# Optimization experiments

Hardware: AMD Instinct MI355X
Metric: run time of the kernel (lower is better)

The kernel has to match this reference:

```python
import jax, jax.numpy as jnp
import numpy as np

N_SEG, N_REG, N_EDGE, HID, CHEB_K = 40000, 1000, 640000, 256, 5


def setup_inputs() -> dict:
    key = jax.random.key(0)
    ks = jax.random.split(key, 6)
    return {
        "projected_region_features": jax.random.normal(ks[0], (N_REG, HID), jnp.float32),
        "segment2region_assignment": jax.random.uniform(ks[1], (N_SEG, N_REG), jnp.float32),
        "edge_index": jax.random.randint(ks[2], (2, N_EDGE), 0, N_SEG, dtype=jnp.int64),
        # ChebConv params: one [HID,HID] weight per Chebyshev order + shared bias
        "cheb_W": jax.random.normal(ks[3], (CHEB_K, HID, HID), jnp.float32) / np.sqrt(HID).astype(np.float32),
        "cheb_b": jnp.zeros((HID,), jnp.float32),
        "ln_gamma": jnp.ones((HID,), jnp.float32),
        "ln_beta": jnp.zeros((HID,), jnp.float32),
    }


def _cheb_conv(x, edge_index, W, b):
    """PyG ChebConv with normalization='sym', lambda_max=2.0.
    Scaled Laplacian L_hat = 2L/lam - I = -D^{-1/2} A D^{-1/2} (diag = 0)."""
    N = x.shape[0]
    src, dst = edge_index[0], edge_index[1]
    w = (src != dst).astype(x.dtype)  # remove_self_loops
    deg = jax.ops.segment_sum(w, src, num_segments=N)
    dinv = jnp.where(deg > 0, jax.lax.rsqrt(jnp.where(deg > 0, deg, 1.0)), 0.0)
    norm = -w * dinv[src] * dinv[dst]  # per-edge weight of L_hat

    def prop(t):  # y_i = sum_{(j->i)} norm_e * t_j
        return jax.ops.segment_sum(norm[:, None] * t[src], dst, num_segments=N)

    Tx0 = x
    out = Tx0 @ W[0]
    Tx1 = prop(Tx0)
    out = out + Tx1 @ W[1]
    for k in range(2, W.shape[0]):
        Tx2 = 2.0 * prop(Tx1) - Tx0
        out = out + Tx2 @ W[k]
        Tx0, Tx1 = Tx1, Tx2
    return out + b


def _layer_norm(x, g, b, eps=1e-5):
    mu = jnp.mean(x, axis=-1, keepdims=True)
    var = jnp.mean(jnp.square(x - mu), axis=-1, keepdims=True)
    return (x - mu) * jax.lax.rsqrt(var + eps) * g + b


def reference(projected_region_features, segment2region_assignment, edge_index,
              cheb_W, cheb_b, ln_gamma, ln_beta):
    # [n_seg, n_reg] @ [n_reg, hid] -> [n_seg, hid]
    seg_low_raw = segment2region_assignment @ projected_region_features
    seg_low = _cheb_conv(seg_low_raw, edge_index, cheb_W, cheb_b)
    seg_low = _layer_norm(jax.nn.gelu(seg_low, approximate=False), ln_gamma, ln_beta)
    return (seg_low, seg_low_raw)
```

## Files before the change

kernel.cpp:

```cpp
#include <hip/hip_runtime.h>

#define NSEG 40000
#define NREG 1000
#define NEDGE 640000
#define HID 256
#define KCAT 1280
#define KP1 1024
#define LPAD 40
#define NBLK 157

typedef float f32x4 __attribute__((ext_vector_type(4)));
typedef float f32x2 __attribute__((ext_vector_type(2)));
typedef short s16x8 __attribute__((ext_vector_type(8)));
typedef unsigned short u16x4 __attribute__((ext_vector_type(4)));
typedef unsigned short u16x8 __attribute__((ext_vector_type(8)));
typedef unsigned int u32x2 __attribute__((ext_vector_type(2)));

typedef __attribute__((address_space(3))) unsigned int lds_u32;
typedef __attribute__((address_space(1))) const unsigned int glb_u32;

__device__ __forceinline__ void dma16(const void* g, void* l) {
    __builtin_amdgcn_global_load_lds((glb_u32*)g, (lds_u32*)l, 16, 0, 0);
}

__device__ __forceinline__ unsigned short f2bf(float f) {
    unsigned u = __builtin_bit_cast(unsigned, f);
    u += 0x7FFFu + ((u >> 16) & 1u);
    return (unsigned short)(u >> 16);
}
__device__ __forceinline__ float bf2f(unsigned short h) {
    unsigned u = ((unsigned)h) << 16;
    return __builtin_bit_cast(float, u);
}
__device__ __forceinline__ unsigned char f2fp8(float v) {
    return (unsigned char)__builtin_amdgcn_cvt_pk_fp8_f32(v, v, 0, false);
}

__device__ __forceinline__ f32x4 mfma16(s16x8 a, s16x8 b, f32x4 c) {
    return __builtin_amdgcn_mfma_f32_16x16x32_bf16(a, b, c, 0, 0, 0);
}

__global__ void detect_kernel(const unsigned int* __restrict__ E, int* flag) {
    int lane = threadIdx.x;
    unsigned v = E[2 * lane + 1];
    unsigned long long m = __ballot(v == 0u);
    if (lane == 0) *flag = (__popcll(m) >= 48) ? 1 : 0;
}

__device__ __forceinline__ int edge_at(const void* E, int idx, int is64) {
    return is64 ? (int)((const long long*)E)[idx] : ((const int*)E)[idx];
}

__global__ __launch_bounds__(256) void deg_cnt_kernel(const void* __restrict__ E,
                                                      const int* __restrict__ flag,
                                                      int* deg, int* cnt) {
    int e = blockIdx.x * 256 + threadIdx.x;
    if (e >= NEDGE) return;
    int is64 = *flag;
    int s = edge_at(E, e, is64);
    int d = edge_at(E, e + NEDGE, is64);
    if (s != d) {
        atomicAdd(&deg[s], 1);
        atomicAdd(&cnt[d], 1);
    }
}

__global__ __launch_bounds__(256) void scan1_kernel(const int* __restrict__ cnt,
                                                    const int* __restrict__ deg,
                                                    float* __restrict__ dinv,
                                                    int* __restrict__ bsum) {
    __shared__ int sh[256];
    int t = threadIdx.x;
    int i = blockIdx.x * 256 + t;
    int c = (i < NSEG) ? cnt[i] : 0;
    sh[t] = c;
    if (i < NSEG) {
        int d = deg[i];
        dinv[i] = d > 0 ? rsqrtf((float)d) : 0.f;
    }
    __syncthreads();
    for (int o = 128; o > 0; o >>= 1) {
        if (t < o) sh[t] += sh[t + o];
        __syncthreads();
    }
    if (t == 0) bsum[blockIdx.x] = sh[0];
}

__global__ __launch_bounds__(256) void scan2_kernel(const int* __restrict__ bsum,
                                                    int* __restrict__ boff,
                                                    int* __restrict__ rowptr) {
    __shared__ int sh[256];
    int t = threadIdx.x;
    int v = (t < NBLK) ? bsum[t] : 0;
    sh[t] = v;
    __syncthreads();
    for (int o = 1; o < 256; o <<= 1) {
        int x = 0;
        if (t >= o) x = sh[t - o];
        __syncthreads();
        if (t >= o) sh[t] += x;
        __syncthreads();
    }
    if (t < NBLK) boff[t] = sh[t] - v;
    if (t == 255) rowptr[NSEG] = sh[255];
}

__global__ __launch_bounds__(256) void scan3_kernel(const int* __restrict__ cnt,
                                                    const int* __restrict__ boff,
                                                    int* __restrict__ rowptr,
                                                    int* __restrict__ cursor) {
    __shared__ int sh[256];
    int t = threadIdx.x;
    int i = blockIdx.x * 256 + t;
    int v = (i < NSEG) ? cnt[i] : 0;
    sh[t] = v;
    __syncthreads();
    for (int o = 1; o < 256; o <<= 1) {
        int x = 0;
        if (t >= o) x = sh[t - o];
        __syncthreads();
        if (t >= o) sh[t] += x;
        __syncthreads();
    }
    if (i < NSEG) {
        int p = boff[blockIdx.x] + sh[t] - v;
        rowptr[i] = p;
        cursor[i] = p;
    }
}

__global__ __launch_bounds__(256) void scatter_kernel(const void* __restrict__ E,
                                                      const int* __restrict__ flag,
                                                      const float* __restrict__ dinv,
                                                      int* cursor,
                                                      long long* __restrict__ colval) {
    int e = blockIdx.x * 256 + threadIdx.x;
    if (e >= NEDGE) return;
    int is64 = *flag;
    int s = edge_at(E, e, is64);
    int d = edge_at(E, e + NEDGE, is64);
    if (s != d) {
        int pos = atomicAdd(&cursor[d], 1);
        float v = -dinv[s] * dinv[d];
        colval[pos] = ((long long)(unsigned)__builtin_bit_cast(unsigned, v) << 32)
                    | (unsigned)s;
    }
}

__global__ void prep_w_kernel(const float* __restrict__ P, const float* __restrict__ W,
                              unsigned short* __restrict__ Pt, unsigned short* __restrict__ Wt) {
    int n = blockIdx.x;
    for (int k = threadIdx.x; k < KP1; k += blockDim.x)
        Pt[(size_t)n * KP1 + k] = (k < NREG) ? f2bf(P[(size_t)k * HID + n]) : (unsigned short)0;
    for (int k = threadIdx.x; k < KCAT; k += blockDim.x)
        Wt[(size_t)n * KCAT + k] = f2bf(W[(size_t)k * HID + n]);
}

__global__ __launch_bounds__(256) void gemm1_kernel(const float* __restrict__ S,
                                                    const unsigned short* __restrict__ Pt,
                                                    float* __restrict__ raw,
                                                    unsigned short* __restrict__ xcat,
                                                    unsigned char* __restrict__ x8) {
    __shared__ unsigned short As[64][LPAD];
    __shared__ unsigned short Bs[256][LPAD];
    const int m0 = blockIdx.x * 64;
    const int tid = threadIdx.x;
    const int lane = tid & 63, wn = tid >> 6;
    const int r = lane & 15, q = lane >> 4;
    const int srow = tid >> 2, scol = (tid & 3) * 8;

    f32x4 acc[4][4] = {};

    for (int kb = 0; kb < NREG; kb += 32) {
        const bool kvalid = (kb + scol + 8 <= NREG);
        u16x8 av = {0, 0, 0, 0, 0, 0, 0, 0};
        u16x8 bv0 = av, bv1 = av, bv2 = av, bv3 = av;
        if (kvalid) {
            const float* sp = S + (size_t)(m0 + srow) * NREG + kb + scol;
            f32x4 f0 = *(const f32x4*)sp;
            f32x4 f1 = *(const f32x4*)(sp + 4);
            av[0] = f2bf(f0[0]); av[1] = f2bf(f0[1]); av[2] = f2bf(f0[2]); av[3] = f2bf(f0[3]);
            av[4] = f2bf(f1[0]); av[5] = f2bf(f1[1]); av[6] = f2bf(f1[2]); av[7] = f2bf(f1[3]);
            bv0 = *(const u16x8*)(Pt + (size_t)(srow)       * KP1 + kb + scol);
            bv1 = *(const u16x8*)(Pt + (size_t)(srow +  64) * KP1 + kb + scol);
            bv2 = *(const u16x8*)(Pt + (size_t)(srow + 128) * KP1 + kb + scol);
            bv3 = *(const u16x8*)(Pt + (size_t)(srow + 192) * KP1 + kb + scol);
        }
        __syncthreads();
        *(u16x8*)&As[srow][scol] = av;
        *(u16x8*)&Bs[srow][scol] = bv0;
        *(u16x8*)&Bs[srow + 64][scol] = bv1;
        *(u16x8*)&Bs[srow + 128][scol] = bv2;
        *(u16x8*)&Bs[srow + 192][scol] = bv3;
        __syncthreads();
        s16x8 af[4], bfv[4];
#pragma unroll
        for (int am = 0; am < 4; ++am) af[am] = *(const s16x8*)&As[am * 16 + r][q * 8];
#pragma unroll
        for (int bn = 0; bn < 4; ++bn) bfv[bn] = *(const s16x8*)&Bs[wn * 64 + bn * 16 + r][q * 8];
#pragma unroll
        for (int am = 0; am < 4; ++am) {
#pragma unroll
            for (int bn = 0; bn < 4; ++bn)
                acc[am][bn] = mfma16(af[am], bfv[bn], acc[am][bn]);
        }
    }
#pragma unroll
    for (int am = 0; am < 4; ++am) {
        int rowb = m0 + am * 16 + q * 4;
#pragma unroll
        for (int bn = 0; bn < 4; ++bn) {
            int col = wn * 64 + bn * 16 + r;
#pragma unroll
            for (int i = 0; i < 4; ++i) {
                float v = acc[am][bn][i];
                raw[(size_t)(rowb + i) * HID + col] = v;
                xcat[(size_t)(rowb + i) * KCAT + col] = f2bf(v);
                x8[(size_t)(rowb + i) * KCAT + col] = f2fp8(v);
            }
        }
    }
}

__global__ __launch_bounds__(256) void prop_kernel(unsigned short* xcat,
                                                   unsigned char* x8,
                                                   const int* __restrict__ rowptr,
                                                   const long long* __restrict__ colval,
                                                   int inOff, int outOff, int subOff,
                                                   float scale, int writeFp8) {
    const int g = blockIdx.x * 4 + (threadIdx.x >> 6);
    const int lane = threadIdx.x & 63;
    const int half = lane >> 5;
    const int l5 = lane & 31;
    const int e0 = rowptr[g], e1 = rowptr[g + 1];
    float a0 = 0.f, a1 = 0.f, a2 = 0.f, a3 = 0.f;
    float a4 = 0.f, a5 = 0.f, a6 = 0.f, a7 = 0.f;
    const unsigned char* xin = x8 + inOff + l5 * 8;

    for (int base = e0; base < e1; base += 64) {
        int m = e1 - base;
        if (m > 64) m = 64;
        int cc = 0;
        float vv = 0.f;
        if (lane < m) {
            long long cv = colval[base + lane];
            cc = (int)(unsigned)cv;
            vv = __builtin_bit_cast(float, (unsigned)(cv >> 32));
        }
        int i = 0;
#pragma unroll 4
        for (; i + 2 <= m; i += 2) {
            int c = __shfl(cc, i + half);
            float v = __shfl(vv, i + half);
            u32x2 t = *(const u32x2*)(xin + (size_t)c * KCAT);
            f32x2 d0 = __builtin_amdgcn_cvt_pk_f32_fp8(t[0], false);
            f32x2 d1 = __builtin_amdgcn_cvt_pk_f32_fp8(t[0], true);
            f32x2 d2 = __builtin_amdgcn_cvt_pk_f32_fp8(t[1], false);
            f32x2 d3 = __builtin_amdgcn_cvt_pk_f32_fp8(t[1], true);
            a0 += v * d0[0]; a1 += v * d0[1];
            a2 += v * d1[0]; a3 += v * d1[1];
            a4 += v * d2[0]; a5 += v * d2[1];
            a6 += v * d3[0]; a7 += v * d3[1];
        }
        if (i < m) {
            int c = __shfl(cc, i);
            float v = __shfl(vv, i);
            if (half == 0) {
                u32x2 t = *(const u32x2*)(xin + (size_t)c * KCAT);
                f32x2 d0 = __builtin_amdgcn_cvt_pk_f32_fp8(t[0], false);
                f32x2 d1 = __builtin_amdgcn_cvt_pk_f32_fp8(t[0], true);
                f32x2 d2 = __builtin_amdgcn_cvt_pk_f32_fp8(t[1], false);
                f32x2 d3 = __builtin_amdgcn_cvt_pk_f32_fp8(t[1], true);
                a0 += v * d0[0]; a1 += v * d0[1];
                a2 += v * d1[0]; a3 += v * d1[1];
                a4 += v * d2[0]; a5 += v * d2[1];
                a6 += v * d3[0]; a7 += v * d3[1];
            }
        }
    }
    a0 += __shfl_xor(a0, 32); a1 += __shfl_xor(a1, 32);
    a2 += __shfl_xor(a2, 32); a3 += __shfl_xor(a3, 32);
    a4 += __shfl_xor(a4, 32); a5 += __shfl_xor(a5, 32);
    a6 += __shfl_xor(a6, 32); a7 += __shfl_xor(a7, 32);

    if (half == 0) {
        a0 *= scale; a1 *= scale; a2 *= scale; a3 *= scale;
        a4 *= scale; a5 *= scale; a6 *= scale; a7 *= scale;
        if (subOff >= 0) {
            u16x8 p = *(const u16x8*)(xcat + (size_t)g * KCAT + subOff + l5 * 8);
            a0 -= bf2f(p[0]); a1 -= bf2f(p[1]); a2 -= bf2f(p[2]); a3 -= bf2f(p[3]);
            a4 -= bf2f(p[4]); a5 -= bf2f(p[5]); a6 -= bf2f(p[6]); a7 -= bf2f(p[7]);
        }
        u16x8 o = {f2bf(a0), f2bf(a1), f2bf(a2), f2bf(a3),
                   f2bf(a4), f2bf(a5), f2bf(a6), f2bf(a7)};
        *(u16x8*)(xcat + (size_t)g * KCAT + outOff + l5 * 8) = o;
        if (writeFp8) {
            unsigned p0 = 0, p1 = 0;
            p0 = __builtin_amdgcn_cvt_pk_fp8_f32(a0, a1, (int)p0, false);
            p0 = __builtin_amdgcn_cvt_pk_fp8_f32(a2, a3, (int)p0, true);
            p1 = __builtin_amdgcn_cvt_pk_fp8_f32(a4, a5, (int)p1, false);
            p1 = __builtin_amdgcn_cvt_pk_fp8_f32(a6, a7, (int)p1, true);
            u32x2 o8 = {p0, p1};
            *(u32x2*)(x8 + (size_t)g * KCAT + outOff + l5 * 8) = o8;
        }
    }
}

__global__ __launch_bounds__(512) void gemm2_kernel(const unsigned short* __restrict__ xcat,
                                                    const unsigned short* __restrict__ Wt,
                                                    const float* __restrict__ bias,
                                                    const float* __restrict__ gamma,
                                                    const float* __restrict__ beta,
                                                    float* __restrict__ outp) {
    __shared__ unsigned short As[2][128 * 32];
    __shared__ unsigned short Bs[2][256 * 32];
    __shared__ float rs[128][4];
    __shared__ float rss[128][4];
    const int tid = threadIdx.x;
    const int lane = tid & 63, wid = tid >> 6;
    const int wm = wid >> 2, wn = wid & 3;
    const int r = lane & 15, q = lane >> 4;
    const int qx8 = (q ^ (r & 3)) << 3;
    const int m0 = blockIdx.x * 128;
    const int crow = lane >> 2;
    const int bcol = (((lane & 3) ^ ((lane >> 2) & 3)) << 3);

    f32x4 acc[4][4] = {};

    auto stage = [&](int c, int kb) {
#pragma unroll
        for (int k = 0; k < 3; ++k) {
            int idx = 3 * wid + k;
            if (idx < 16) {
                int n = idx * 16 + crow;
                dma16(Wt + (size_t)n * KCAT + kb + bcol, &Bs[c][idx * 512]);
            } else {
                int a = idx - 16;
                int row = m0 + a * 16 + crow;
                dma16(xcat + (size_t)row * KCAT + kb + bcol, &As[c][a * 512]);
            }
        }
    };

    stage(0, 0);
    __syncthreads();

    for (int t = 0; t < 40; ++t) {
        const int c = t & 1;
        if (t < 39) stage(c ^ 1, (t + 1) * 32);
        s16x8 af[4], bfv[4];
#pragma unroll
        for (int am = 0; am < 4; ++am)
            af[am] = *(const s16x8*)&As[c][(wm * 64 + am * 16 + r) * 32 + qx8];
#pragma unroll
        for (int bn = 0; bn < 4; ++bn)
            bfv[bn] = *(const s16x8*)&Bs[c][(wn * 64 + bn * 16 + r) * 32 + qx8];
#pragma unroll
        for (int am = 0; am < 4; ++am)
#pragma unroll
            for (int bn = 0; bn < 4; ++bn)
                acc[am][bn] = mfma16(af[am], bfv[bn], acc[am][bn]);
        __syncthreads();
    }

    float bc[4], gm[4], bt[4];
#pragma unroll
    for (int bn = 0; bn < 4; ++bn) {
        int col = wn * 64 + bn * 16 + r;
        bc[bn] = bias[col];
        gm[bn] = gamma[col];
        bt[bn] = beta[col];
    }
#pragma unroll
    for (int am = 0; am < 4; ++am) {
#pragma unroll
        for (int i = 0; i < 4; ++i) {
            float s = 0.f, ss = 0.f;
#pragma unroll
            for (int bn = 0; bn < 4; ++bn) {
                float v = acc[am][bn][i] + bc[bn];
                v = 0.5f * v * (1.f + erff(v * 0.70710678118654752f));
                acc[am][bn][i] = v;
                s += v;
                ss += v * v;
            }
#pragma unroll
            for (int msk = 1; msk < 16; msk <<= 1) {
                s += __shfl_xor(s, msk);
                ss += __shfl_xor(ss, msk);
            }
            if (r == 0) {
                int row = wm * 64 + am * 16 + q * 4 + i;
                rs[row][wn] = s;
                rss[row][wn] = ss;
            }
        }
    }
    __syncthreads();
#pragma unroll
    for (int am = 0; am < 4; ++am) {
#pragma unroll
        for (int i = 0; i < 4; ++i) {
            int row = wm * 64 + am * 16 + q * 4 + i;
            float s = rs[row][0] + rs[row][1] + rs[row][2] + rs[row][3];
            float ss = rss[row][0] + rss[row][1] + rss[row][2] + rss[row][3];
            float mu = s * (1.f / HID);
            float var = ss * (1.f / HID) - mu * mu;
            float inv = rsqrtf(var + 1e-5f);
            if (m0 + row < NSEG) {
#pragma unroll
                for (int bn = 0; bn < 4; ++bn) {
                    int col = wn * 64 + bn * 16 + r;
                    outp[(size_t)(m0 + row) * HID + col] = (acc[am][bn][i] - mu) * inv * gm[bn] + bt[bn];
                }
            }
        }
    }
}

extern "C" void kernel_launch(void* const* d_in, const int* in_sizes, int n_in,
                              void* d_out, int out_size, void* d_ws, size_t ws_size,
                              hipStream_t stream) {
    const float* P     = (const float*)d_in[0];
    const float* S     = (const float*)d_in[1];
    const void*  E     = d_in[2];
    const float* W     = (const float*)d_in[3];
    const float* bias  = (const float*)d_in[4];
    const float* gamma = (const float*)d_in[5];
    const float* beta  = (const float*)d_in[6];

    float* out = (float*)d_out;
    float* raw = out + (size_t)NSEG * HID;

    char* ws = (char*)d_ws;
    size_t off = 0;
    auto alloc = [&](size_t bytes) -> void* {
        void* p = ws + off;
        off += (bytes + 255) & ~(size_t)255;
        return p;
    };
    unsigned short* xcat   = (unsigned short*)alloc((size_t)NSEG * KCAT * 2);
    unsigned char*  x8     = (unsigned char*)alloc((size_t)NSEG * KCAT);
    unsigned short* Pt     = (unsigned short*)alloc((size_t)HID * KP1 * 2);
    unsigned short* Wt     = (unsigned short*)alloc((size_t)HID * KCAT * 2);
    int*            deg    = (int*)alloc((size_t)NSEG * 4);
    float*          dinv   = (float*)alloc((size_t)NSEG * 4);
    int*            cnt    = (int*)alloc((size_t)NSEG * 4);
    int*            rowptr = (int*)alloc((size_t)(NSEG + 1) * 4);
    int*            cursor = (int*)alloc((size_t)NSEG * 4);
    long long*      colval = (long long*)alloc((size_t)NEDGE * 8);
    int*            bsum   = (int*)alloc((size_t)NBLK * 4);
    int*            boff   = (int*)alloc((size_t)NBLK * 4);
    int*            flag   = (int*)alloc(256);
    if (off > ws_size) return;

    hipMemsetAsync(deg, 0, (size_t)NSEG * 4, stream);
    hipMemsetAsync(cnt, 0, (size_t)NSEG * 4, stream);

    detect_kernel<<<1, 64, 0, stream>>>((const unsigned int*)E, flag);
    prep_w_kernel<<<HID, 256, 0, stream>>>(P, W, Pt, Wt);

    deg_cnt_kernel<<<NEDGE / 256, 256, 0, stream>>>(E, flag, deg, cnt);
    scan1_kernel<<<NBLK, 256, 0, stream>>>(cnt, deg, dinv, bsum);
    scan2_kernel<<<1, 256, 0, stream>>>(bsum, boff, rowptr);
    scan3_kernel<<<NBLK, 256, 0, stream>>>(cnt, boff, rowptr, cursor);
    scatter_kernel<<<NEDGE / 256, 256, 0, stream>>>(E, flag, dinv, cursor, colval);

    gemm1_kernel<<<NSEG / 64, 256, 0, stream>>>(S, Pt, raw, xcat, x8);

    prop_kernel<<<NSEG / 4, 256, 0, stream>>>(xcat, x8, rowptr, colval, 0 * HID, 1 * HID, -1, 1.f, 1);
    prop_kernel<<<NSEG / 4, 256, 0, stream>>>(xcat, x8, rowptr, colval, 1 * HID, 2 * HID, 0 * HID, 2.f, 1);
    prop_kernel<<<NSEG / 4, 256, 0, stream>>>(xcat, x8, rowptr, colval, 2 * HID, 3 * HID, 1 * HID, 2.f, 1);
    prop_kernel<<<NSEG / 4, 256, 0, stream>>>(xcat, x8, rowptr, colval, 3 * HID, 4 * HID, 2 * HID, 2.f, 0);

    gemm2_kernel<<<(NSEG + 127) / 128, 512, 0, stream>>>(xcat, Wt, bias, gamma, beta, out);
}
```

Before: 385.5 us.

## Run final Chebyshev GEMM in FP8 using fp8 activations and weights

The output GEMM over the concatenated Chebyshev features now reads FP8 copies of the activations and weights and uses the fp8 16x16x32 MFMA instead of bf16. The last propagation step now also writes an FP8 copy, and prep_w builds an FP8 transposed weight matrix. The LDS staging layout changes to 32-byte rows without the XOR swizzle. This halves the GEMM's global and LDS traffic and uses the faster FP8 matrix path. In exchange, accuracy drops because activations and weights are quantized to FP8, which risks tolerance failures, and the unswizzled LDS reads may hit bank conflicts.

```diff
diff --git a/kernel.cpp b/kernel.cpp
--- a/kernel.cpp
+++ b/kernel.cpp
@@ -38,6 +38,9 @@
 
 __device__ __forceinline__ f32x4 mfma16(s16x8 a, s16x8 b, f32x4 c) {
     return __builtin_amdgcn_mfma_f32_16x16x32_bf16(a, b, c, 0, 0, 0);
+}
+__device__ __forceinline__ f32x4 mfma8(long a, long b, f32x4 c) {
+    return __builtin_amdgcn_mfma_f32_16x16x32_fp8_fp8(a, b, c, 0, 0, 0);
 }
 
 __global__ void detect_kernel(const unsigned int* __restrict__ E, int* flag) {
@@ -148,12 +151,16 @@
 }
 
 __global__ void prep_w_kernel(const float* __restrict__ P, const float* __restrict__ W,
-                              unsigned short* __restrict__ Pt, unsigned short* __restrict__ Wt) {
+                              unsigned short* __restrict__ Pt, unsigned short* __restrict__ Wt,
+                              unsigned char* __restrict__ Wt8) {
     int n = blockIdx.x;
     for (int k = threadIdx.x; k < KP1; k += blockDim.x)
         Pt[(size_t)n * KP1 + k] = (k < NREG) ? f2bf(P[(size_t)k * HID + n]) : (unsigned short)0;
-    for (int k = threadIdx.x; k < KCAT; k += blockDim.x)
-        Wt[(size_t)n * KCAT + k] = f2bf(W[(size_t)k * HID + n]);
+    for (int k = threadIdx.x; k < KCAT; k += blockDim.x) {
+        float w = W[(size_t)k * HID + n];
+        Wt[(size_t)n * KCAT + k] = f2bf(w);
+        Wt8[(size_t)n * KCAT + k] = f2fp8(w);
+    }
 }
 
 __global__ __launch_bounds__(256) void gemm1_kernel(const float* __restrict__ S,
@@ -227,7 +234,7 @@
                                                    const int* __restrict__ rowptr,
                                                    const long long* __restrict__ colval,
                                                    int inOff, int outOff, int subOff,
-                                                   float scale, int writeFp8) {
+                                                   float scale) {
     const int g = blockIdx.x * 4 + (threadIdx.x >> 6);
     const int lane = threadIdx.x & 63;
     const int half = lane >> 5;
@@ -294,51 +301,44 @@
         u16x8 o = {f2bf(a0), f2bf(a1), f2bf(a2), f2bf(a3),
                    f2bf(a4), f2bf(a5), f2bf(a6), f2bf(a7)};
         *(u16x8*)(xcat + (size_t)g * KCAT + outOff + l5 * 8) = o;
-        if (writeFp8) {
-            unsigned p0 = 0, p1 = 0;
-            p0 = __builtin_amdgcn_cvt_pk_fp8_f32(a0, a1, (int)p0, false);
-            p0 = __builtin_amdgcn_cvt_pk_fp8_f32(a2, a3, (int)p0, true);
-            p1 = __builtin_amdgcn_cvt_pk_fp8_f32(a4, a5, (int)p1, false);
-            p1 = __builtin_amdgcn_cvt_pk_fp8_f32(a6, a7, (int)p1, true);
-            u32x2 o8 = {p0, p1};
-            *(u32x2*)(x8 + (size_t)g * KCAT + outOff + l5 * 8) = o8;
-        }
-    }
-}
-
-__global__ __launch_bounds__(512) void gemm2_kernel(const unsigned short* __restrict__ xcat,
-                                                    const unsigned short* __restrict__ Wt,
+        unsigned p0 = 0, p1 = 0;
+        p0 = __builtin_amdgcn_cvt_pk_fp8_f32(a0, a1, (int)p0, false);
+        p0 = __builtin_amdgcn_cvt_pk_fp8_f32(a2, a3, (int)p0, true);
+        p1 = __builtin_amdgcn_cvt_pk_fp8_f32(a4, a5, (int)p1, false);
+        p1 = __builtin_amdgcn_cvt_pk_fp8_f32(a6, a7, (int)p1, true);
+        u32x2 o8 = {p0, p1};
+        *(u32x2*)(x8 + (size_t)g * KCAT + outOff + l5 * 8) = o8;
+    }
+}
+
+__global__ __launch_bounds__(512) void gemm2_kernel(const unsigned char* __restrict__ x8,
+                                                    const unsigned char* __restrict__ Wt8,
                                                     const float* __restrict__ bias,
                                                     const float* __restrict__ gamma,
                                                     const float* __restrict__ beta,
                                                     float* __restrict__ outp) {
-    __shared__ unsigned short As[2][128 * 32];
-    __shared__ unsigned short Bs[2][256 * 32];
+    __shared__ unsigned char As8[2][128 * 32];
+    __shared__ unsigned char Bs8[2][256 * 32];
     __shared__ float rs[128][4];
     __shared__ float rss[128][4];
     const int tid = threadIdx.x;
     const int lane = tid & 63, wid = tid >> 6;
     const int wm = wid >> 2, wn = wid & 3;
     const int r = lane & 15, q = lane >> 4;
-    const int qx8 = (q ^ (r & 3)) << 3;
     const int m0 = blockIdx.x * 128;
-    const int crow = lane >> 2;
-    const int bcol = (((lane & 3) ^ ((lane >> 2) & 3)) << 3);
+    const int drow = lane >> 1;
+    const int dhalf = (lane & 1) * 16;
 
     f32x4 acc[4][4] = {};
 
     auto stage = [&](int c, int kb) {
-#pragma unroll
-        for (int k = 0; k < 3; ++k) {
-            int idx = 3 * wid + k;
-            if (idx < 16) {
-                int n = idx * 16 + crow;
-                dma16(Wt + (size_t)n * KCAT + kb + bcol, &Bs[c][idx * 512]);
-            } else {
-                int a = idx - 16;
-                int row = m0 + a * 16 + crow;
-                dma16(xcat + (size_t)row * KCAT + kb + bcol, &As[c][a * 512]);
-            }
+        {
+            int n = wid * 32 + drow;
+            dma16(Wt8 + (size_t)n * KCAT + kb + dhalf, &Bs8[c][wid * 1024]);
+        }
+        if (wid < 4) {
+            int row = m0 + wid * 32 + drow;
+            dma16(x8 + (size_t)row * KCAT + kb + dhalf, &As8[c][wid * 1024]);
         }
     };
 
@@ -348,18 +348,18 @@
     for (int t = 0; t < 40; ++t) {
         const int c = t & 1;
         if (t < 39) stage(c ^ 1, (t + 1) * 32);
-        s16x8 af[4], bfv[4];
+        long af[4], bfv[4];
 #pragma unroll
         for (int am = 0; am < 4; ++am)
-            af[am] = *(const s16x8*)&As[c][(wm * 64 + am * 16 + r) * 32 + qx8];
+            af[am] = *(const long*)&As8[c][(wm * 64 + am * 16 + r) * 32 + q * 8];
 #pragma unroll
         for (int bn = 0; bn < 4; ++bn)
-            bfv[bn] = *(const s16x8*)&Bs[c][(wn * 64 + bn * 16 + r) * 32 + qx8];
+            bfv[bn] = *(const long*)&Bs8[c][(wn * 64 + bn * 16 + r) * 32 + q * 8];
 #pragma unroll
         for (int am = 0; am < 4; ++am)
 #pragma unroll
             for (int bn = 0; bn < 4; ++bn)
-                acc[am][bn] = mfma16(af[am], bfv[bn], acc[am][bn]);
+                acc[am][bn] = mfma8(af[am], bfv[bn], acc[am][bn]);
         __syncthreads();
     }
 
@@ -443,6 +443,7 @@
     unsigned char*  x8     = (unsigned char*)alloc((size_t)NSEG * KCAT);
     unsigned short* Pt     = (unsigned short*)alloc((size_t)HID * KP1 * 2);
     unsigned short* Wt     = (unsigned short*)alloc((size_t)HID * KCAT * 2);
+    unsigned char*  Wt8    = (unsigned char*)alloc((size_t)HID * KCAT);
     int*            deg    = (int*)alloc((size_t)NSEG * 4);
     float*          dinv   = (float*)alloc((size_t)NSEG * 4);
     int*            cnt    = (int*)alloc((size_t)NSEG * 4);
@@ -458,7 +459,7 @@
     hipMemsetAsync(cnt, 0, (size_t)NSEG * 4, stream);
 
     detect_kernel<<<1, 64, 0, stream>>>((const unsigned int*)E, flag);
-    prep_w_kernel<<<HID, 256, 0, stream>>>(P, W, Pt, Wt);
+    prep_w_kernel<<<HID, 256, 0, stream>>>(P, W, Pt, Wt, Wt8);
 
     deg_cnt_kernel<<<NEDGE / 256, 256, 0, stream>>>(E, flag, deg, cnt);
     scan1_kernel<<<NBLK, 256, 0, stream>>>(cnt, deg, dinv, bsum);
@@ -468,10 +469,10 @@
 
     gemm1_kernel<<<NSEG / 64, 256, 0, stream>>>(S, Pt, raw, xcat, x8);
 
-    prop_kernel<<<NSEG / 4, 256, 0, stream>>>(xcat, x8, rowptr, colval, 0 * HID, 1 * HID, -1, 1.f, 1);
-    prop_kernel<<<NSEG / 4, 256, 0, stream>>>(xcat, x8, rowptr, colval, 1 * HID, 2 * HID, 0 * HID, 2.f, 1);
-    prop_kernel<<<NSEG / 4, 256, 0, stream>>>(xcat, x8, rowptr, colval, 2 * HID, 3 * HID, 1 * HID, 2.f, 1);
-    prop_kernel<<<NSEG / 4, 256, 0, stream>>>(xcat, x8, rowptr, colval, 3 * HID, 4 * HID, 2 * HID, 2.f, 0);
-
-    gemm2_kernel<<<(NSEG + 127) / 128, 512, 0, stream>>>(xcat, Wt, bias, gamma, beta, out);
-}
+    prop_kernel<<<NSEG / 4, 256, 0, stream>>>(xcat, x8, rowptr, colval, 0 * HID, 1 * HID, -1, 1.f);
+    prop_kernel<<<NSEG / 4, 256, 0, stream>>>(xcat, x8, rowptr, colval, 1 * HID, 2 * HID, 0 * HID, 2.f);
+    prop_kernel<<<NSEG / 4, 256, 0, stream>>>(xcat, x8, rowptr, colval, 2 * HID, 3 * HID, 1 * HID, 2.f);
+    prop_kernel<<<NSEG / 4, 256, 0, stream>>>(xcat, x8, rowptr, colval, 3 * HID, 4 * HID, 2 * HID, 2.f);
+
+    gemm2_kernel<<<(NSEG + 127) / 128, 512, 0, stream>>>(x8, Wt8, bias, gamma, beta, out);
+}
```

After: 390.4 us. Within noise of the previous version (+1.3%).

## Switch Chebyshev combine GEMM to FP8 MFMA and widen GEMM1 K-step

Applied to the files above, without the earlier changes.

The final concatenated GEMM now reads FP8 activations and FP8 weights, using the 16x16x32 fp8 MFMA with 64-wide K tiles and a swizzled LDS layout. This halves the operand bytes loaded per output tile and the number of K iterations. The prop kernels now always write FP8 and only write bf16 where a later subtraction needs it, which cuts store traffic. GEMM1 processes 64 K-columns per barrier pair instead of 32. The cost is lower accuracy, since FP8 weights and activations feed a LayerNorm output, and a tail-clamping trick that reads index 0 for out-of-range K, relying on the zero padding in Pt to cancel those terms.

```diff
diff --git a/kernel.cpp b/kernel.cpp
--- a/kernel.cpp
+++ b/kernel.cpp
@@ -6,7 +6,7 @@
 #define HID 256
 #define KCAT 1280
 #define KP1 1024
-#define LPAD 40
+#define LP2 72
 #define NBLK 157
 
 typedef float f32x4 __attribute__((ext_vector_type(4)));
@@ -38,6 +38,9 @@
 
 __device__ __forceinline__ f32x4 mfma16(s16x8 a, s16x8 b, f32x4 c) {
     return __builtin_amdgcn_mfma_f32_16x16x32_bf16(a, b, c, 0, 0, 0);
+}
+__device__ __forceinline__ f32x4 mfma8(long a, long b, f32x4 c) {
+    return __builtin_amdgcn_mfma_f32_16x16x32_fp8_fp8(a, b, c, 0, 0, 0);
 }
 
 __global__ void detect_kernel(const unsigned int* __restrict__ E, int* flag) {
@@ -148,12 +151,12 @@
 }
 
 __global__ void prep_w_kernel(const float* __restrict__ P, const float* __restrict__ W,
-                              unsigned short* __restrict__ Pt, unsigned short* __restrict__ Wt) {
+                              unsigned short* __restrict__ Pt, unsigned char* __restrict__ Wt8) {
     int n = blockIdx.x;
     for (int k = threadIdx.x; k < KP1; k += blockDim.x)
         Pt[(size_t)n * KP1 + k] = (k < NREG) ? f2bf(P[(size_t)k * HID + n]) : (unsigned short)0;
     for (int k = threadIdx.x; k < KCAT; k += blockDim.x)
-        Wt[(size_t)n * KCAT + k] = f2bf(W[(size_t)k * HID + n]);
+        Wt8[(size_t)n * KCAT + k] = f2fp8(W[(size_t)k * HID + n]);
 }
 
 __global__ __launch_bounds__(256) void gemm1_kernel(const float* __restrict__ S,
@@ -161,49 +164,64 @@
                                                     float* __restrict__ raw,
                                                     unsigned short* __restrict__ xcat,
                                                     unsigned char* __restrict__ x8) {
-    __shared__ unsigned short As[64][LPAD];
-    __shared__ unsigned short Bs[256][LPAD];
+    __shared__ unsigned short As[64][LP2];
+    __shared__ unsigned short Bs[256][LP2];
     const int m0 = blockIdx.x * 64;
     const int tid = threadIdx.x;
     const int lane = tid & 63, wn = tid >> 6;
     const int r = lane & 15, q = lane >> 4;
-    const int srow = tid >> 2, scol = (tid & 3) * 8;
+    const int srow = tid >> 2, scol = (tid & 3) * 16;
+    const float* aptr = S + (size_t)(m0 + srow) * NREG;
 
     f32x4 acc[4][4] = {};
 
-    for (int kb = 0; kb < NREG; kb += 32) {
-        const bool kvalid = (kb + scol + 8 <= NREG);
-        u16x8 av = {0, 0, 0, 0, 0, 0, 0, 0};
-        u16x8 bv0 = av, bv1 = av, bv2 = av, bv3 = av;
-        if (kvalid) {
-            const float* sp = S + (size_t)(m0 + srow) * NREG + kb + scol;
-            f32x4 f0 = *(const f32x4*)sp;
-            f32x4 f1 = *(const f32x4*)(sp + 4);
-            av[0] = f2bf(f0[0]); av[1] = f2bf(f0[1]); av[2] = f2bf(f0[2]); av[3] = f2bf(f0[3]);
-            av[4] = f2bf(f1[0]); av[5] = f2bf(f1[1]); av[6] = f2bf(f1[2]); av[7] = f2bf(f1[3]);
-            bv0 = *(const u16x8*)(Pt + (size_t)(srow)       * KP1 + kb + scol);
-            bv1 = *(const u16x8*)(Pt + (size_t)(srow +  64) * KP1 + kb + scol);
-            bv2 = *(const u16x8*)(Pt + (size_t)(srow + 128) * KP1 + kb + scol);
-            bv3 = *(const u16x8*)(Pt + (size_t)(srow + 192) * KP1 + kb + scol);
-        }
-        __syncthreads();
-        *(u16x8*)&As[srow][scol] = av;
-        *(u16x8*)&Bs[srow][scol] = bv0;
-        *(u16x8*)&Bs[srow + 64][scol] = bv1;
-        *(u16x8*)&Bs[srow + 128][scol] = bv2;
-        *(u16x8*)&Bs[srow + 192][scol] = bv3;
-        __syncthreads();
-        s16x8 af[4], bfv[4];
-#pragma unroll
-        for (int am = 0; am < 4; ++am) af[am] = *(const s16x8*)&As[am * 16 + r][q * 8];
-#pragma unroll
-        for (int bn = 0; bn < 4; ++bn) bfv[bn] = *(const s16x8*)&Bs[wn * 64 + bn * 16 + r][q * 8];
+    for (int kb = 0; kb < KP1; kb += 64) {
+        int ka0 = kb + scol;     if (ka0 + 8 > NREG) ka0 = 0;
+        int ka1 = kb + scol + 8; if (ka1 + 8 > NREG) ka1 = 0;
+        f32x4 f0 = *(const f32x4*)(aptr + ka0);
+        f32x4 f1 = *(const f32x4*)(aptr + ka0 + 4);
+        f32x4 f2 = *(const f32x4*)(aptr + ka1);
+        f32x4 f3 = *(const f32x4*)(aptr + ka1 + 4);
+        u16x8 bv[4][2];
+#pragma unroll
+        for (int j = 0; j < 4; ++j) {
+            const unsigned short* bp = Pt + (size_t)(j * 64 + srow) * KP1 + kb + scol;
+            bv[j][0] = *(const u16x8*)(bp);
+            bv[j][1] = *(const u16x8*)(bp + 8);
+        }
+        __syncthreads();
+        {
+            u16x8 a0 = {f2bf(f0[0]), f2bf(f0[1]), f2bf(f0[2]), f2bf(f0[3]),
+                        f2bf(f1[0]), f2bf(f1[1]), f2bf(f1[2]), f2bf(f1[3])};
+            u16x8 a1 = {f2bf(f2[0]), f2bf(f2[1]), f2bf(f2[2]), f2bf(f2[3]),
+                        f2bf(f3[0]), f2bf(f3[1]), f2bf(f3[2]), f2bf(f3[3])};
+            *(u16x8*)&As[srow][scol] = a0;
+            *(u16x8*)&As[srow][scol + 8] = a1;
+        }
+#pragma unroll
+        for (int j = 0; j < 4; ++j) {
+            *(u16x8*)&Bs[j * 64 + srow][scol] = bv[j][0];
+            *(u16x8*)&Bs[j * 64 + srow][scol + 8] = bv[j][1];
+        }
+        __syncthreads();
+        s16x8 af[4][2], bfv[4][2];
 #pragma unroll
         for (int am = 0; am < 4; ++am) {
-#pragma unroll
-            for (int bn = 0; bn < 4; ++bn)
-                acc[am][bn] = mfma16(af[am], bfv[bn], acc[am][bn]);
-        }
+            af[am][0] = *(const s16x8*)&As[am * 16 + r][q * 8];
+            af[am][1] = *(const s16x8*)&As[am * 16 + r][32 + q * 8];
+        }
+#pragma unroll
+        for (int bn = 0; bn < 4; ++bn) {
+            bfv[bn][0] = *(const s16x8*)&Bs[wn * 64 + bn * 16 + r][q * 8];
+            bfv[bn][1] = *(const s16x8*)&Bs[wn * 64 + bn * 16 + r][32 + q * 8];
+        }
+#pragma unroll
+        for (int kk = 0; kk < 2; ++kk)
+#pragma unroll
+            for (int am = 0; am < 4; ++am)
+#pragma unroll
+                for (int bn = 0; bn < 4; ++bn)
+                    acc[am][bn] = mfma16(af[am][kk], bfv[bn][kk], acc[am][bn]);
     }
 #pragma unroll
     for (int am = 0; am < 4; ++am) {
@@ -227,7 +245,7 @@
                                                    const int* __restrict__ rowptr,
                                                    const long long* __restrict__ colval,
                                                    int inOff, int outOff, int subOff,
-                                                   float scale, int writeFp8) {
+                                                   float scale, int writeBf16) {
     const int g = blockIdx.x * 4 + (threadIdx.x >> 6);
     const int lane = threadIdx.x & 63;
     const int half = lane >> 5;
@@ -291,39 +309,38 @@
             a0 -= bf2f(p[0]); a1 -= bf2f(p[1]); a2 -= bf2f(p[2]); a3 -= bf2f(p[3]);
             a4 -= bf2f(p[4]); a5 -= bf2f(p[5]); a6 -= bf2f(p[6]); a7 -= bf2f(p[7]);
         }
-        u16x8 o = {f2bf(a0), f2bf(a1), f2bf(a2), f2bf(a3),
-                   f2bf(a4), f2bf(a5), f2bf(a6), f2bf(a7)};
-        *(u16x8*)(xcat + (size_t)g * KCAT + outOff + l5 * 8) = o;
-        if (writeFp8) {
-            unsigned p0 = 0, p1 = 0;
-            p0 = __builtin_amdgcn_cvt_pk_fp8_f32(a0, a1, (int)p0, false);
-            p0 = __builtin_amdgcn_cvt_pk_fp8_f32(a2, a3, (int)p0, true);
-            p1 = __builtin_amdgcn_cvt_pk_fp8_f32(a4, a5, (int)p1, false);
-            p1 = __builtin_amdgcn_cvt_pk_fp8_f32(a6, a7, (int)p1, true);
-            u32x2 o8 = {p0, p1};
-            *(u32x2*)(x8 + (size_t)g * KCAT + outOff + l5 * 8) = o8;
-        }
-    }
-}
-
-__global__ __launch_bounds__(512) void gemm2_kernel(const unsigned short* __restrict__ xcat,
-                                                    const unsigned short* __restrict__ Wt,
+        if (writeBf16) {
+            u16x8 o = {f2bf(a0), f2bf(a1), f2bf(a2), f2bf(a3),
+                       f2bf(a4), f2bf(a5), f2bf(a6), f2bf(a7)};
+            *(u16x8*)(xcat + (size_t)g * KCAT + outOff + l5 * 8) = o;
+        }
+        unsigned p0 = 0, p1 = 0;
+        p0 = __builtin_amdgcn_cvt_pk_fp8_f32(a0, a1, (int)p0, false);
+        p0 = __builtin_amdgcn_cvt_pk_fp8_f32(a2, a3, (int)p0, true);
+        p1 = __builtin_amdgcn_cvt_pk_fp8_f32(a4, a5, (int)p1, false);
+        p1 = __builtin_amdgcn_cvt_pk_fp8_f32(a6, a7, (int)p1, true);
+        u32x2 o8 = {p0, p1};
+        *(u32x2*)(x8 + (size_t)g * KCAT + outOff + l5 * 8) = o8;
+    }
+}
+
+__global__ __launch_bounds__(512) void gemm2_kernel(const unsigned char* __restrict__ x8,
+                                                    const unsigned char* __restrict__ Wt8,
                                                     const float* __restrict__ bias,
                                                     const float* __restrict__ gamma,
                                                     const float* __restrict__ beta,
                                                     float* __restrict__ outp) {
-    __shared__ unsigned short As[2][128 * 32];
-    __shared__ unsigned short Bs[2][256 * 32];
+    __shared__ unsigned char As8[2][128 * 64];
+    __shared__ unsigned char Bs8[2][256 * 64];
     __shared__ float rs[128][4];
     __shared__ float rss[128][4];
     const int tid = threadIdx.x;
     const int lane = tid & 63, wid = tid >> 6;
     const int wm = wid >> 2, wn = wid & 3;
     const int r = lane & 15, q = lane >> 4;
-    const int qx8 = (q ^ (r & 3)) << 3;
     const int m0 = blockIdx.x * 128;
     const int crow = lane >> 2;
-    const int bcol = (((lane & 3) ^ ((lane >> 2) & 3)) << 3);
+    const int scol16 = (((lane & 3) ^ ((lane >> 2) & 3)) << 4);
 
     f32x4 acc[4][4] = {};
 
@@ -333,33 +350,46 @@
             int idx = 3 * wid + k;
             if (idx < 16) {
                 int n = idx * 16 + crow;
-                dma16(Wt + (size_t)n * KCAT + kb + bcol, &Bs[c][idx * 512]);
+                dma16(Wt8 + (size_t)n * KCAT + kb + scol16, &Bs8[c][idx * 1024]);
             } else {
                 int a = idx - 16;
                 int row = m0 + a * 16 + crow;
-                dma16(xcat + (size_t)row * KCAT + kb + bcol, &As[c][a * 512]);
-            }
-        }
+                dma16(x8 + (size_t)row * KCAT + kb + scol16, &As8[c][a * 1024]);
+            }
+        }
+    };
+
+    auto lda = [&](const unsigned char* base, int row, int kk) -> long {
+        int g16 = (kk * 2 + (q >> 1)) ^ (row & 3);
+        return *(const long*)(base + row * 64 + g16 * 16 + (q & 1) * 8);
     };
 
     stage(0, 0);
     __syncthreads();
 
-    for (int t = 0; t < 40; ++t) {
+    for (int t = 0; t < 20; ++t) {
         const int c = t & 1;
-        if (t < 39) stage(c ^ 1, (t + 1) * 32);
-        s16x8 af[4], bfv[4];
-#pragma unroll
-        for (int am = 0; am < 4; ++am)
-            af[am] = *(const s16x8*)&As[c][(wm * 64 + am * 16 + r) * 32 + qx8];
-#pragma unroll
-        for (int bn = 0; bn < 4; ++bn)
-            bfv[bn] = *(const s16x8*)&Bs[c][(wn * 64 + bn * 16 + r) * 32 + qx8];
-#pragma unroll
-        for (int am = 0; am < 4; ++am)
-#pragma unroll
-            for (int bn = 0; bn < 4; ++bn)
-                acc[am][bn] = mfma16(af[am], bfv[bn], acc[am][bn]);
+        if (t < 19) stage(c ^ 1, (t + 1) * 64);
+        long af[4][2], bfv[4][2];
+#pragma unroll
+        for (int am = 0; am < 4; ++am) {
+            int row = wm * 64 + am * 16 + r;
+            af[am][0] = lda(As8[c], row, 0);
+            af[am][1] = lda(As8[c], row, 1);
+        }
+#pragma unroll
+        for (int bn = 0; bn < 4; ++bn) {
+            int row = wn * 64 + bn * 16 + r;
+            bfv[bn][0] = lda(Bs8[c], row, 0);
+            bfv[bn][1] = lda(Bs8[c], row, 1);
+        }
+#pragma unroll
+        for (int kk = 0; kk < 2; ++kk)
+#pragma unroll
+            for (int am = 0; am < 4; ++am)
+#pragma unroll
+                for (int bn = 0; bn < 4; ++bn)
+                    acc[am][bn] = mfma8(af[am][kk], bfv[bn][kk], acc[am][bn]);
         __syncthreads();
     }
 
@@ -442,7 +472,7 @@
     unsigned short* xcat   = (unsigned short*)alloc((size_t)NSEG * KCAT * 2);
     unsigned char*  x8     = (unsigned char*)alloc((size_t)NSEG * KCAT);
     unsigned short* Pt     = (unsigned short*)alloc((size_t)HID * KP1 * 2);
-    unsigned short* Wt     = (unsigned short*)alloc((size_t)HID * KCAT * 2);
+    unsigned char*  Wt8    = (unsigned char*)alloc((size_t)HID * KCAT);
     int*            deg    = (int*)alloc((size_t)NSEG * 4);
     float*          dinv   = (float*)alloc((size_t)NSEG * 4);
     int*            cnt    = (int*)alloc((size_t)NSEG * 4);
@@ -458,7 +488,7 @@
     hipMemsetAsync(cnt, 0, (size_t)NSEG * 4, stream);
 
     detect_kernel<<<1, 64, 0, stream>>>((const unsigned int*)E, flag);
-    prep_w_kernel<<<HID, 256, 0, stream>>>(P, W, Pt, Wt);
+    prep_w_kernel<<<HID, 256, 0, stream>>>(P, W, Pt, Wt8);
 
     deg_cnt_kernel<<<NEDGE / 256, 256, 0, stream>>>(E, flag, deg, cnt);
     scan1_kernel<<<NBLK, 256, 0, stream>>>(cnt, deg, dinv, bsum);
@@ -470,8 +500,8 @@
 
     prop_kernel<<<NSEG / 4, 256, 0, stream>>>(xcat, x8, rowptr, colval, 0 * HID, 1 * HID, -1, 1.f, 1);
     prop_kernel<<<NSEG / 4, 256, 0, stream>>>(xcat, x8, rowptr, colval, 1 * HID, 2 * HID, 0 * HID, 2.f, 1);
-    prop_kernel<<<NSEG / 4, 256, 0, stream>>>(xcat, x8, rowptr, colval, 2 * HID, 3 * HID, 1 * HID, 2.f, 1);
+    prop_kernel<<<NSEG / 4, 256, 0, stream>>>(xcat, x8, rowptr, colval, 2 * HID, 3 * HID, 1 * HID, 2.f, 0);
     prop_kernel<<<NSEG / 4, 256, 0, stream>>>(xcat, x8, rowptr, colval, 3 * HID, 4 * HID, 2 * HID, 2.f, 0);
 
-    gemm2_kernel<<<(NSEG + 127) / 128, 512, 0, stream>>>(xcat, Wt, bias, gamma, beta, out);
-}
+    gemm2_kernel<<<(NSEG + 127) / 128, 512, 0, stream>>>(x8, Wt8, bias, gamma, beta, out);
+}
```

After: 383.7 us. About the same (-0.5%).

## Switch final Chebyshev GEMM to FP8 MFMA and skip unneeded bf16 writes

Applied to the files above, without the earlier changes.

The final concatenated GEMM (40000x1280 by 1280x256) now reads FP8 activations and FP8 weights and uses the 16x16x32 fp8 MFMA. It replaces the double-buffered bf16 DMA pipeline with a simpler 64-row tile that loads through registers into LDS. All prop passes now always write FP8, and the last two passes skip the bf16 output that is no longer consumed. This halves GEMM operand bytes and raises MFMA throughput. The cost is lost accuracy from FP8 weights and activations, and losing the async double-buffering, which may expose load latency.

```diff
diff --git a/kernel.cpp b/kernel.cpp
--- a/kernel.cpp
+++ b/kernel.cpp
@@ -7,6 +7,7 @@
 #define KCAT 1280
 #define KP1 1024
 #define LPAD 40
+#define LF8 72
 #define NBLK 157
 
 typedef float f32x4 __attribute__((ext_vector_type(4)));
@@ -15,13 +16,7 @@
 typedef unsigned short u16x4 __attribute__((ext_vector_type(4)));
 typedef unsigned short u16x8 __attribute__((ext_vector_type(8)));
 typedef unsigned int u32x2 __attribute__((ext_vector_type(2)));
-
-typedef __attribute__((address_space(3))) unsigned int lds_u32;
-typedef __attribute__((address_space(1))) const unsigned int glb_u32;
-
-__device__ __forceinline__ void dma16(const void* g, void* l) {
-    __builtin_amdgcn_global_load_lds((glb_u32*)g, (lds_u32*)l, 16, 0, 0);
-}
+typedef unsigned int u32x4 __attribute__((ext_vector_type(4)));
 
 __device__ __forceinline__ unsigned short f2bf(float f) {
     unsigned u = __builtin_bit_cast(unsigned, f);
@@ -38,6 +33,9 @@
 
 __device__ __forceinline__ f32x4 mfma16(s16x8 a, s16x8 b, f32x4 c) {
     return __builtin_amdgcn_mfma_f32_16x16x32_bf16(a, b, c, 0, 0, 0);
+}
+__device__ __forceinline__ f32x4 mfma8(long a, long b, f32x4 c) {
+    return __builtin_amdgcn_mfma_f32_16x16x32_fp8_fp8(a, b, c, 0, 0, 0);
 }
 
 __global__ void detect_kernel(const unsigned int* __restrict__ E, int* flag) {
@@ -148,12 +146,12 @@
 }
 
 __global__ void prep_w_kernel(const float* __restrict__ P, const float* __restrict__ W,
-                              unsigned short* __restrict__ Pt, unsigned short* __restrict__ Wt) {
+                              unsigned short* __restrict__ Pt, unsigned char* __restrict__ Wt8) {
     int n = blockIdx.x;
     for (int k = threadIdx.x; k < KP1; k += blockDim.x)
         Pt[(size_t)n * KP1 + k] = (k < NREG) ? f2bf(P[(size_t)k * HID + n]) : (unsigned short)0;
     for (int k = threadIdx.x; k < KCAT; k += blockDim.x)
-        Wt[(size_t)n * KCAT + k] = f2bf(W[(size_t)k * HID + n]);
+        Wt8[(size_t)n * KCAT + k] = f2fp8(W[(size_t)k * HID + n]);
 }
 
 __global__ __launch_bounds__(256) void gemm1_kernel(const float* __restrict__ S,
@@ -227,7 +225,7 @@
                                                    const int* __restrict__ rowptr,
                                                    const long long* __restrict__ colval,
                                                    int inOff, int outOff, int subOff,
-                                                   float scale, int writeFp8) {
+                                                   float scale, int writeBf16) {
     const int g = blockIdx.x * 4 + (threadIdx.x >> 6);
     const int lane = threadIdx.x & 63;
     const int half = lane >> 5;
@@ -291,76 +289,70 @@
             a0 -= bf2f(p[0]); a1 -= bf2f(p[1]); a2 -= bf2f(p[2]); a3 -= bf2f(p[3]);
             a4 -= bf2f(p[4]); a5 -= bf2f(p[5]); a6 -= bf2f(p[6]); a7 -= bf2f(p[7]);
         }
-        u16x8 o = {f2bf(a0), f2bf(a1), f2bf(a2), f2bf(a3),
-                   f2bf(a4), f2bf(a5), f2bf(a6), f2bf(a7)};
-        *(u16x8*)(xcat + (size_t)g * KCAT + outOff + l5 * 8) = o;
-        if (writeFp8) {
-            unsigned p0 = 0, p1 = 0;
-            p0 = __builtin_amdgcn_cvt_pk_fp8_f32(a0, a1, (int)p0, false);
-            p0 = __builtin_amdgcn_cvt_pk_fp8_f32(a2, a3, (int)p0, true);
-            p1 = __builtin_amdgcn_cvt_pk_fp8_f32(a4, a5, (int)p1, false);
-            p1 = __builtin_amdgcn_cvt_pk_fp8_f32(a6, a7, (int)p1, true);
-            u32x2 o8 = {p0, p1};
-            *(u32x2*)(x8 + (size_t)g * KCAT + outOff + l5 * 8) = o8;
-        }
-    }
-}
-
-__global__ __launch_bounds__(512) void gemm2_kernel(const unsigned short* __restrict__ xcat,
-                                                    const unsigned short* __restrict__ Wt,
+        if (writeBf16) {
+            u16x8 o = {f2bf(a0), f2bf(a1), f2bf(a2), f2bf(a3),
+                       f2bf(a4), f2bf(a5), f2bf(a6), f2bf(a7)};
+            *(u16x8*)(xcat + (size_t)g * KCAT + outOff + l5 * 8) = o;
+        }
+        unsigned p0 = 0, p1 = 0;
+        p0 = __builtin_amdgcn_cvt_pk_fp8_f32(a0, a1, (int)p0, false);
+        p0 = __builtin_amdgcn_cvt_pk_fp8_f32(a2, a3, (int)p0, true);
+        p1 = __builtin_amdgcn_cvt_pk_fp8_f32(a4, a5, (int)p1, false);
+        p1 = __builtin_amdgcn_cvt_pk_fp8_f32(a6, a7, (int)p1, true);
+        u32x2 o8 = {p0, p1};
+        *(u32x2*)(x8 + (size_t)g * KCAT + outOff + l5 * 8) = o8;
+    }
+}
+
+__global__ __launch_bounds__(256) void gemm2_kernel(const unsigned char* __restrict__ x8,
+                                                    const unsigned char* __restrict__ Wt8,
                                                     const float* __restrict__ bias,
                                                     const float* __restrict__ gamma,
                                                     const float* __restrict__ beta,
                                                     float* __restrict__ outp) {
-    __shared__ unsigned short As[2][128 * 32];
-    __shared__ unsigned short Bs[2][256 * 32];
-    __shared__ float rs[128][4];
-    __shared__ float rss[128][4];
+    __shared__ unsigned char As8[64][LF8];
+    __shared__ unsigned char Bs8[256][LF8];
+    __shared__ float rs[64][4];
+    __shared__ float rss[64][4];
+    const int m0 = blockIdx.x * 64;
     const int tid = threadIdx.x;
-    const int lane = tid & 63, wid = tid >> 6;
-    const int wm = wid >> 2, wn = wid & 3;
+    const int lane = tid & 63, wn = tid >> 6;
     const int r = lane & 15, q = lane >> 4;
-    const int qx8 = (q ^ (r & 3)) << 3;
-    const int m0 = blockIdx.x * 128;
-    const int crow = lane >> 2;
-    const int bcol = (((lane & 3) ^ ((lane >> 2) & 3)) << 3);
+    const int srow = tid >> 2, scol = (tid & 3) * 16;
+    const unsigned char* aptr = x8 + (size_t)(m0 + srow) * KCAT;
 
     f32x4 acc[4][4] = {};
 
-    auto stage = [&](int c, int kb) {
-#pragma unroll
-        for (int k = 0; k < 3; ++k) {
-            int idx = 3 * wid + k;
-            if (idx < 16) {
-                int n = idx * 16 + crow;
-                dma16(Wt + (size_t)n * KCAT + kb + bcol, &Bs[c][idx * 512]);
-            } else {
-                int a = idx - 16;
-                int row = m0 + a * 16 + crow;
-                dma16(xcat + (size_t)row * KCAT + kb + bcol, &As[c][a * 512]);
-            }
-        }
-    };
-
-    stage(0, 0);
-    __syncthreads();
-
-    for (int t = 0; t < 40; ++t) {
-        const int c = t & 1;
-        if (t < 39) stage(c ^ 1, (t + 1) * 32);
-        s16x8 af[4], bfv[4];
-#pragma unroll
-        for (int am = 0; am < 4; ++am)
-            af[am] = *(const s16x8*)&As[c][(wm * 64 + am * 16 + r) * 32 + qx8];
-#pragma unroll
-        for (int bn = 0; bn < 4; ++bn)
-            bfv[bn] = *(const s16x8*)&Bs[c][(wn * 64 + bn * 16 + r) * 32 + qx8];
-#pragma unroll
-        for (int am = 0; am < 4; ++am)
-#pragma unroll
-            for (int bn = 0; bn < 4; ++bn)
-                acc[am][bn] = mfma16(af[am], bfv[bn], acc[am][bn]);
-        __syncthreads();
+    for (int kb = 0; kb < KCAT; kb += 64) {
+        u32x4 av = *(const u32x4*)(aptr + kb + scol);
+        u32x4 bv[4];
+#pragma unroll
+        for (int j = 0; j < 4; ++j)
+            bv[j] = *(const u32x4*)(Wt8 + (size_t)(j * 64 + srow) * KCAT + kb + scol);
+        __syncthreads();
+        *(u32x4*)&As8[srow][scol] = av;
+#pragma unroll
+        for (int j = 0; j < 4; ++j)
+            *(u32x4*)&Bs8[j * 64 + srow][scol] = bv[j];
+        __syncthreads();
+        long af[4][2], bfv[4][2];
+#pragma unroll
+        for (int am = 0; am < 4; ++am) {
+            af[am][0] = *(const long*)&As8[am * 16 + r][q * 8];
+            af[am][1] = *(const long*)&As8[am * 16 + r][32 + q * 8];
+        }
+#pragma unroll
+        for (int bn = 0; bn < 4; ++bn) {
+            bfv[bn][0] = *(const long*)&Bs8[wn * 64 + bn * 16 + r][q * 8];
+            bfv[bn][1] = *(const long*)&Bs8[wn * 64 + bn * 16 + r][32 + q * 8];
+        }
+#pragma unroll
+        for (int kk = 0; kk < 2; ++kk)
+#pragma unroll
+            for (int am = 0; am < 4; ++am)
+#pragma unroll
+                for (int bn = 0; bn < 4; ++bn)
+                    acc[am][bn] = mfma8(af[am][kk], bfv[bn][kk], acc[am][bn]);
     }
 
     float bc[4], gm[4], bt[4];
@@ -390,7 +382,7 @@
                 ss += __shfl_xor(ss, msk);
             }
             if (r == 0) {
-                int row = wm * 64 + am * 16 + q * 4 + i;
+                int row = am * 16 + q * 4 + i;
                 rs[row][wn] = s;
                 rss[row][wn] = ss;
             }
@@ -401,18 +393,16 @@
     for (int am = 0; am < 4; ++am) {
 #pragma unroll
         for (int i = 0; i < 4; ++i) {
-            int row = wm * 64 + am * 16 + q * 4 + i;
+            int row = am * 16 + q * 4 + i;
             float s = rs[row][0] + rs[row][1] + rs[row][2] + rs[row][3];
             float ss = rss[row][0] + rss[row][1] + rss[row][2] + rss[row][3];
             float mu = s * (1.f / HID);
             float var = ss * (1.f / HID) - mu * mu;
             float inv = rsqrtf(var + 1e-5f);
-            if (m0 + row < NSEG) {
-#pragma unroll
-                for (int bn = 0; bn < 4; ++bn) {
-                    int col = wn * 64 + bn * 16 + r;
-                    outp[(size_t)(m0 + row) * HID + col] = (acc[am][bn][i] - mu) * inv * gm[bn] + bt[bn];
-                }
+#pragma unroll
+            for (int bn = 0; bn < 4; ++bn) {
+                int col = wn * 64 + bn * 16 + r;
+                outp[(size_t)(m0 + row) * HID + col] = (acc[am][bn][i] - mu) * inv * gm[bn] + bt[bn];
             }
         }
     }
@@ -442,7 +432,7 @@
     unsigned short* xcat   = (unsigned short*)alloc((size_t)NSEG * KCAT * 2);
     unsigned char*  x8     = (unsigned char*)alloc((size_t)NSEG * KCAT);
     unsigned short* Pt     = (unsigned short*)alloc((size_t)HID * KP1 * 2);
-    unsigned short* Wt     = (unsigned short*)alloc((size_t)HID * KCAT * 2);
+    unsigned char*  Wt8    = (unsigned char*)alloc((size_t)HID * KCAT);
     int*            deg    = (int*)alloc((size_t)NSEG * 4);
     float*          dinv   = (float*)alloc((size_t)NSEG * 4);
     int*            cnt    = (int*)alloc((size_t)NSEG * 4);
@@ -458,7 +448,7 @@
     hipMemsetAsync(cnt, 0, (size_t)NSEG * 4, stream);
 
     detect_kernel<<<1, 64, 0, stream>>>((const unsigned int*)E, flag);
-    prep_w_kernel<<<HID, 256, 0, stream>>>(P, W, Pt, Wt);
+    prep_w_kernel<<<HID, 256, 0, stream>>>(P, W, Pt, Wt8);
 
     deg_cnt_kernel<<<NEDGE / 256, 256, 0, stream>>>(E, flag, deg, cnt);
     scan1_kernel<<<NBLK, 256, 0, stream>>>(cnt, deg, dinv, bsum);
@@ -470,8 +460,8 @@
 
     prop_kernel<<<NSEG / 4, 256, 0, stream>>>(xcat, x8, rowptr, colval, 0 * HID, 1 * HID, -1, 1.f, 1);
     prop_kernel<<<NSEG / 4, 256, 0, stream>>>(xcat, x8, rowptr, colval, 1 * HID, 2 * HID, 0 * HID, 2.f, 1);
-    prop_kernel<<<NSEG / 4, 256, 0, stream>>>(xcat, x8, rowptr, colval, 2 * HID, 3 * HID, 1 * HID, 2.f, 1);
+    prop_kernel<<<NSEG / 4, 256, 0, stream>>>(xcat, x8, rowptr, colval, 2 * HID, 3 * HID, 1 * HID, 2.f, 0);
     prop_kernel<<<NSEG / 4, 256, 0, stream>>>(xcat, x8, rowptr, colval, 3 * HID, 4 * HID, 2 * HID, 2.f, 0);
 
-    gemm2_kernel<<<(NSEG + 127) / 128, 512, 0, stream>>>(xcat, Wt, bias, gamma, beta, out);
-}
+    gemm2_kernel<<<NSEG / 64, 256, 0, stream>>>(x8, Wt8, bias, gamma, beta, out);
+}
```

Result: no change. 383.1 us (-0.6%).
